# Kernel optimization log

Measured on AMD Instinct MI355X. Metric: run time of the kernel, lower is better.

The kernel has to match this reference:

```python
import jax, jax.numpy as jnp
import numpy as np

EPS = 1e-7  # K.epsilon()

def squash(v, axis=-1):
    s2 = jnp.sum(jnp.square(v), axis=axis, keepdims=True)
    scale = s2 / (1.0 + s2) / jnp.sqrt(s2 + EPS)
    return scale * v

def setup_inputs() -> dict:
    key = jax.random.key(0)
    k1, k2 = jax.random.split(key)
    B, N, D_in = 128, 2048, 8
    J, P = 32, 16
    x = jax.random.normal(k1, (B, N, D_in), dtype=jnp.float32)
    W = jax.random.normal(k2, (J, N, P, D_in), dtype=jnp.float32) * 0.05
    return {"x": x, "W": W}

def reference(x, W):
    # x: [B, N, D_in]; W: [J, N, P, D_in]
    routings = 3
    J = W.shape[0]
    # inputs_hat: [B, J, N, P] -- u_hat_{j|n} = W_{jn} @ u_n
    inputs_hat = jnp.einsum('bni,jnpi->bjnp', x, W)
    B, _, N, _ = inputs_hat.shape
    b = jnp.zeros((B, J, N), dtype=inputs_hat.dtype)
    outputs = None
    for i in range(routings):
        c = jax.nn.softmax(b, axis=1)  # softmax over output capsules J
        s = jnp.einsum('bjn,bjnp->bjp', c, inputs_hat)
        outputs = squash(s)  # [B, J, P]
        if i < routings - 1:
            b = b + jnp.einsum('bjp,bjnp->bjn', outputs, inputs_hat)
    return outputs
```

## Files before the change

### kernel.cpp

```cpp
#include <hip/hip_runtime.h>
#include <math.h>

constexpr int Bb = 128;
constexpr int Nn = 2048;
constexpr int Dd = 8;
constexpr int Jj = 32;
constexpr int Pp = 16;

constexpr int BT = 2;
constexpr int WV = 8;
constexpr int BB = BT * WV;
constexpr int BN = 32;
constexpr int NBC = Bb / BB;
constexpr int NNC = Nn / BN;
constexpr int GRID = NBC * NNC;
constexpr int SZ = Bb * Jj * Pp;
constexpr size_t W16_ELEMS = (size_t)Jj * Nn * Pp * Dd;

typedef _Float16 half2v __attribute__((ext_vector_type(2)));
typedef _Float16 half8  __attribute__((ext_vector_type(8)));
typedef float    floatx4 __attribute__((ext_vector_type(4)));

#if __has_builtin(__builtin_amdgcn_fdot2)
__device__ inline float fdot2(half2v a, half2v b, float c) {
    return __builtin_amdgcn_fdot2(a, b, c, false);
}
#else
__device__ inline float fdot2(half2v a, half2v b, float c) {
    return (float)a.x * (float)b.x + (float)a.y * (float)b.y + c;
}
#endif

__device__ inline half2v bch2(unsigned u) { return __builtin_bit_cast(half2v, u); }
__device__ inline half8  bch8(uint4 u)    { return __builtin_bit_cast(half8, u); }
__device__ inline unsigned pkh2(float lo, float hi) {
    half2v h; h.x = (_Float16)lo; h.y = (_Float16)hi;
    return __builtin_bit_cast(unsigned, h);
}

__global__ __launch_bounds__(256)
void w16cvt_k(const float* __restrict__ W, ushort* __restrict__ W16)
{
    const size_t g = (size_t)blockIdx.x * 256 + threadIdx.x;
    const float4* Wg = reinterpret_cast<const float4*>(W);
    float4 a = Wg[2 * g], b = Wg[2 * g + 1];
    uint4 o;
    o.x = pkh2(a.x, a.y); o.y = pkh2(a.z, a.w);
    o.z = pkh2(b.x, b.y); o.w = pkh2(b.z, b.w);
    reinterpret_cast<uint4*>(W16)[g] = o;
}

__global__ __launch_bounds__(512, 4)
void gemm0_v3(const float* __restrict__ x, const ushort* __restrict__ W16,
              float* __restrict__ S)
{
    __shared__ uint4 xl[32 * 128];

    const int tid  = threadIdx.x;
    const int wave = tid >> 6;
    const int lane = tid & 63;

    const int id  = blockIdx.x;
    const int xcd = id & 7;
    const int rem = id >> 3;
    const int jpc = rem & 7;
    const int nch = rem >> 3;
    const int nc  = xcd + 8 * nch;
    const int jp0 = jpc * 64;
    const int n0  = nc * 32;

    {
        const int xb = tid >> 2, xq = tid & 3;
        const float4* Xg = reinterpret_cast<const float4*>(x);
        #pragma unroll
        for (int r = 0; r < 8; ++r) {
            const int nn = r * 4 + xq;
            const size_t base = ((size_t)xb * 2048 + n0 + nn) * 2;
            float4 a = Xg[base], b = Xg[base + 1];
            uint4 o;
            o.x = pkh2(a.x, a.y); o.y = pkh2(a.z, a.w);
            o.z = pkh2(b.x, b.y); o.w = pkh2(b.z, b.w);
            xl[nn * 128 + xb] = o;
        }
    }
    __syncthreads();

    const int ar = lane & 15;
    const int kg = lane >> 4;

    const uint4* W16v = reinterpret_cast<const uint4*>(W16);
    const size_t abase = ((size_t)(jpc * 4) * 2048 + n0 + kg) * 16 + ar;

    floatx4 acc[4];
    #pragma unroll
    for (int f = 0; f < 4; ++f)
        #pragma unroll
        for (int q = 0; q < 4; ++q) acc[f][q] = 0.f;

    #pragma unroll
    for (int ks = 0; ks < 8; ++ks) {
        half8 bfrag = bch8(xl[(ks * 4 + kg) * 128 + wave * 16 + ar]);
        #pragma unroll
        for (int f = 0; f < 4; ++f) {
            half8 afrag = bch8(W16v[abase + (size_t)f * 2048 * 16 + (size_t)ks * 4 * 16]);
            acc[f] = __builtin_amdgcn_mfma_f32_16x16x32_f16(afrag, bfrag, acc[f], 0, 0, 0);
        }
    }

    float* outp = S + (size_t)nc * SZ;
    const int bcol = wave * 16 + ar;
    #pragma unroll
    for (int f = 0; f < 4; ++f) {
        const size_t off = (size_t)bcol * 512 + jp0 + f * 16 + kg * 4;
        *reinterpret_cast<float4*>(outp + off) =
            make_float4(acc[f][0], acc[f][1], acc[f][2], acc[f][3]);
    }
}

__global__ __launch_bounds__(512, 4)
void route_m(const float* __restrict__ x, const ushort* __restrict__ W16,
             const float* __restrict__ OS, float* __restrict__ S)
{
    __shared__ uint4 xl[16 * 32];
    __shared__ float pl[2][512];

    const int tid  = threadIdx.x;
    const int w    = tid >> 6;
    const int lane = tid & 63;
    const int ar   = lane & 15;
    const int kg   = lane >> 4;

    const int id  = blockIdx.x;
    const int xcd = id & 7;
    const int bc  = (id >> 3) & 7;
    const int nch = id >> 6;
    const int nc  = xcd + 8 * nch;
    const int b0  = bc * 16;
    const int n0  = nc * 32;

    {
        const int b = tid >> 5, n = tid & 31;
        const float4* src = reinterpret_cast<const float4*>(
            x + ((size_t)(b0 + b) * Nn + n0 + n) * Dd);
        float4 a = src[0], c4 = src[1];
        uint4 o;
        o.x = pkh2(a.x, a.y);  o.y = pkh2(a.z, a.w);
        o.z = pkh2(c4.x, c4.y); o.w = pkh2(c4.z, c4.w);
        xl[n * 16 + ((b + n) & 15)] = o;
    }

    float4 o4[4];
    {
        const float4* osv = reinterpret_cast<const float4*>(OS);
        #pragma unroll
        for (int f = 0; f < 4; ++f)
            o4[f] = osv[((size_t)(b0 + ar) * Jj + (w * 4 + f)) * 4 + kg];
    }

    float Sa[4][4];
    #pragma unroll
    for (int f = 0; f < 4; ++f)
        #pragma unroll
        for (int q = 0; q < 4; ++q) Sa[f][q] = 0.f;

    const uint4* W16v = reinterpret_cast<const uint4*>(W16);

    __syncthreads();

    uint4 aw[4];
    #pragma unroll
    for (int f = 0; f < 4; ++f)
        aw[f] = W16v[((size_t)(w * 4 + f) * Nn + n0 + kg) * 16 + ar];

    const half8 hz = {};

    for (int g = 0; g < 8; ++g) {
        const int nl = g * 4;

        half8 bfull = bch8(xl[(nl + kg) * 16 + ((ar + nl + kg) & 15)]);

        floatx4 res[4][4];
        #pragma unroll
        for (int s = 0; s < 4; ++s) {
            half8 bs = (kg == s) ? bfull : hz;
            #pragma unroll
            for (int f = 0; f < 4; ++f) {
                floatx4 z = {0.f, 0.f, 0.f, 0.f};
                res[f][s] = __builtin_amdgcn_mfma_f32_16x16x32_f16(bch8(aw[f]), bs, z, 0, 0, 0);
            }
        }

        if (g < 7) {
            #pragma unroll
            for (int f = 0; f < 4; ++f)
                aw[f] = W16v[((size_t)(w * 4 + f) * Nn + n0 + nl + 4 + kg) * 16 + ar];
        }

        float efs0 = 0.f, efs1 = 0.f, efs2 = 0.f, efs3 = 0.f;
        #pragma unroll
        for (int f = 0; f < 4; ++f) {
            #pragma unroll
            for (int s = 0; s < 4; ++s) {
                float lg = o4[f].x * res[f][s][0];
                lg = fmaf(o4[f].y, res[f][s][1], lg);
                lg = fmaf(o4[f].z, res[f][s][2], lg);
                lg = fmaf(o4[f].w, res[f][s][3], lg);
                lg += __shfl_xor(lg, 16, 64);
                lg += __shfl_xor(lg, 32, 64);
                float ee = __expf(lg);
                res[f][s] = res[f][s] * ee;
                if (s == 0) efs0 += ee; else if (s == 1) efs1 += ee;
                else if (s == 2) efs2 += ee; else efs3 += ee;
            }
        }

        float t01 = (kg & 1) ? efs1 : efs0;
        float t23 = (kg & 1) ? efs3 : efs2;
        float myp = (kg & 2) ? t23 : t01;
        pl[g & 1][w * 64 + lane] = myp;
        __syncthreads();

        float se = 0.f;
        #pragma unroll
        for (int ww = 0; ww < 8; ++ww) se += pl[g & 1][ww * 64 + lane];
        float rse = __builtin_amdgcn_rcpf(se);

        float r1 = __shfl_xor(rse, 16, 64);
        float r2 = __shfl_xor(rse, 32, 64);
        float r3 = __shfl_xor(r1, 32, 64);
        float rs[4];
        #pragma unroll
        for (int s = 0; s < 4; ++s) {
            float a01 = ((s ^ kg) & 1) ? r1 : rse;
            float a23 = ((s ^ kg) & 1) ? r3 : r2;
            rs[s] = ((s ^ kg) & 2) ? a23 : a01;
        }

        #pragma unroll
        for (int f = 0; f < 4; ++f) {
            #pragma unroll
            for (int s = 0; s < 4; ++s) {
                #pragma unroll
                for (int q = 0; q < 4; ++q)
                    Sa[f][q] = fmaf(rs[s], res[f][s][q], Sa[f][q]);
            }
        }
    }

    float* outp = S + (size_t)nc * SZ + (size_t)(b0 + ar) * 512;
    #pragma unroll
    for (int f = 0; f < 4; ++f) {
        *reinterpret_cast<float4*>(outp + (w * 4 + f) * 16 + kg * 4) =
            make_float4(Sa[f][0], Sa[f][1], Sa[f][2], Sa[f][3]);
    }
}

template<int WT>
__global__ __launch_bounds__(512, 2)
void gemm0_k2(const float* __restrict__ x, const float* __restrict__ W,
              ushort* __restrict__ W16, float* __restrict__ S)
{
    __shared__ uint4 wl[2][256];
    __shared__ uint4 xl[2][512];

    const int tid  = threadIdx.x;
    const int wave = tid >> 6;
    const int lane = tid & 63;

    const int id  = blockIdx.x;
    const int xcd = id & 7;
    const int rem = id >> 3;
    const int jpc = rem & 7;
    const int nch = rem >> 3;
    const int nc  = xcd + 8 * nch;
    const int jp0 = jpc * 64;
    const int n0  = nc * 32;

    const int wns = (tid >> 6) & 3;
    const int wjpr = tid & 63;
    const int wjp = jp0 + wjpr, wj = wjp >> 4, wp = wjp & 15;
    const int xb = tid >> 2, xq = tid & 3;

    const float4* Wg = reinterpret_cast<const float4*>(W);
    const float4* Xg = reinterpret_cast<const float4*>(x);
    uint4* W16v = reinterpret_cast<uint4*>(W16);

    float4 wa, wb2, xa, xb2;
    auto load_t = [&](int ks) {
        const int n = n0 + ks * 4;
        if (tid < 256) {
            const size_t base = ((size_t)wj * 2048 + (n + wns)) * 32 + wp * 2;
            wa = Wg[base]; wb2 = Wg[base + 1];
        }
        const size_t xbase = ((size_t)xb * 2048 + n) * 2 + xq * 2;
        xa = Xg[xbase]; xb2 = Xg[xbase + 1];
    };
    auto store_t = [&](int buf, int ks) {
        if (tid < 256) {
            uint4 o;
            o.x = pkh2(wa.x, wa.y);   o.y = pkh2(wa.z, wa.w);
            o.z = pkh2(wb2.x, wb2.y); o.w = pkh2(wb2.z, wb2.w);
            wl[buf][tid] = o;
            if (WT)
                W16v[((size_t)wj * 2048 + (n0 + ks * 4 + wns)) * 16 + wp] = o;
        }
        uint4 o2;
        o2.x = pkh2(xa.x, xa.y);   o2.y = pkh2(xa.z, xa.w);
        o2.z = pkh2(xb2.x, xb2.y); o2.w = pkh2(xb2.z, xb2.w);
        xl[buf][xq * 128 + xb] = o2;
    };

    floatx4 acc[4];
    #pragma unroll
    for (int f = 0; f < 4; ++f)
        #pragma unroll
        for (int q = 0; q < 4; ++q) acc[f][q] = 0.f;

    load_t(0);
    store_t(0, 0);
    __syncthreads();

    const int kg = lane >> 4;
    const int ar = lane & 15;

    for (int ks = 0; ks < 8; ++ks) {
        if (ks < 7) load_t(ks + 1);
        const int buf = ks & 1;

        half8 bfrag = bch8(xl[buf][kg * 128 + wave * 16 + ar]);
        #pragma unroll
        for (int f = 0; f < 4; ++f) {
            half8 afrag = bch8(wl[buf][kg * 64 + f * 16 + ar]);
            acc[f] = __builtin_amdgcn_mfma_f32_16x16x32_f16(afrag, bfrag, acc[f], 0, 0, 0);
        }

        if (ks < 7) {
            store_t(buf ^ 1, ks + 1);
            __syncthreads();
        }
    }

    float* outp = S + (size_t)nc * SZ;
    const int bcol = wave * 16 + ar;
    #pragma unroll
    for (int f = 0; f < 4; ++f) {
        const size_t off = (size_t)bcol * 512 + jp0 + f * 16 + kg * 4;
        *reinterpret_cast<float4*>(outp + off) =
            make_float4(acc[f][0], acc[f][1], acc[f][2], acc[f][3]);
    }
}

template<int LOGITS, int ATOMIC, int W16F>
__global__ __launch_bounds__(512, 4)
void route_k(const float* __restrict__ x, const float* __restrict__ W,
             const ushort* __restrict__ W16,
             const float* __restrict__ OS, float* __restrict__ S)
{
    __shared__ uint4 wbuf[2][512];
    __shared__ uint4 xs[BB * BN];

    const int tid  = threadIdx.x;
    const int wave = tid >> 6;
    const int lane = tid & 63;

    const int id  = blockIdx.x;
    const int xcd = id & 7;
    const int bc  = (id >> 3) & 7;
    const int nch = id >> 6;
    const int nc  = xcd + 8 * nch;
    const int b0  = bc * BB;
    const int n0  = nc * BN;
    const int j   = lane >> 1;
    const int hp  = lane & 1;

    {
        const int b = tid >> 5, n = tid & 31;
        const float4* src = reinterpret_cast<const float4*>(
            x + ((size_t)(b0 + b) * Nn + n0 + n) * Dd);
        float4 a = src[0], c4 = src[1];
        uint4 o;
        o.x = pkh2(a.x, a.y);  o.y = pkh2(a.z, a.w);
        o.z = pkh2(c4.x, c4.y); o.w = pkh2(c4.z, c4.w);
        xs[b * BN + n] = o;
    }

    const float4* Wg = reinterpret_cast<const float4*>(W);
    const int sj = tid >> 4;
    const int sp = tid & 15;
    const int sl = sj * 2 + (sp >> 3);
    const int spp = sp & 7;
    const int wslot = spp * 64 + ((sl + spp) & 63);
    const int ispp = tid >> 6;
    const int isl  = ((tid & 63) - ispp) & 63;
    const int isj  = isl >> 1;
    const int isp  = ((isl & 1) << 3) | ispp;
    const uint4* W16v = reinterpret_cast<const uint4*>(W16);
    const size_t wbase16 = (size_t)isj * 32768 + isp;

    float4 sta, stb;
    uint4 st16;
    auto load_slice = [&](int n) {
        if (W16F) {
            st16 = W16v[wbase16 + (size_t)n * 16];
        } else {
            const size_t base = (size_t)n * 32 + sp * 2 + (size_t)sj * ((size_t)Nn * 32);
            sta = Wg[base];
            stb = Wg[base + 1];
        }
    };
    auto store_slice = [&](int buf) {
        if (W16F) {
            wbuf[buf][tid] = st16;
        } else {
            uint4 o;
            o.x = pkh2(sta.x, sta.y);  o.y = pkh2(sta.z, sta.w);
            o.z = pkh2(stb.x, stb.y);  o.w = pkh2(stb.z, stb.w);
            wbuf[buf][wslot] = o;
        }
    };

    float osum[BT][8];
    if (LOGITS) {
        #pragma unroll
        for (int bb = 0; bb < BT; ++bb) {
            const float4* op = reinterpret_cast<const float4*>(
                OS + ((size_t)(b0 + wave * BT + bb) * Jj + j) * Pp + hp * 8);
            float4 a = op[0], b4 = op[1];
            osum[bb][0] = a.x;  osum[bb][1] = a.y;  osum[bb][2] = a.z;  osum[bb][3] = a.w;
            osum[bb][4] = b4.x; osum[bb][5] = b4.y; osum[bb][6] = b4.z; osum[bb][7] = b4.w;
        }
    }

    float Sa[BT][8];
    #pragma unroll
    for (int bb = 0; bb < BT; ++bb)
        #pragma unroll
        for (int pp = 0; pp < 8; ++pp) Sa[bb][pp] = 0.f;

    load_slice(n0);
    store_slice(0);
    __syncthreads();

    const uint4* xw = xs + (size_t)(wave * BT) * BN;

    for (int nn = 0; nn < BN; ++nn) {
        if (nn + 1 < BN) load_slice(n0 + nn + 1);
        const int buf = nn & 1;

        half2v x01[BT], x23[BT], x45[BT], x67[BT];
        #pragma unroll
        for (int bb = 0; bb < BT; ++bb) {
            uint4 xr = xw[(size_t)bb * BN + nn];
            x01[bb] = bch2(xr.x); x23[bb] = bch2(xr.y);
            x45[bb] = bch2(xr.z); x67[bb] = bch2(xr.w);
        }

        float uh[BT][8];
        #pragma unroll
        for (int pp = 0; pp < 8; ++pp) {
            uint4 wv = wbuf[buf][pp * 64 + ((lane + pp) & 63)];
            half2v w01 = bch2(wv.x), w23 = bch2(wv.y);
            half2v w45 = bch2(wv.z), w67 = bch2(wv.w);
            #pragma unroll
            for (int bb = 0; bb < BT; ++bb) {
                float acc = fdot2(w01, x01[bb], 0.f);
                acc = fdot2(w23, x23[bb], acc);
                acc = fdot2(w45, x45[bb], acc);
                acc = fdot2(w67, x67[bb], acc);
                uh[bb][pp] = acc;
            }
        }

        if (!LOGITS) {
            #pragma unroll
            for (int bb = 0; bb < BT; ++bb)
                #pragma unroll
                for (int pp = 0; pp < 8; ++pp) Sa[bb][pp] += uh[bb][pp];
        } else {
            #pragma unroll
            for (int bb = 0; bb < BT; ++bb) {
                float lg = 0.f;
                #pragma unroll
                for (int pp = 0; pp < 8; ++pp)
                    lg = fmaf(osum[bb][pp], uh[bb][pp], lg);
                lg += __shfl_xor(lg, 1, 64);
                float e = __expf(lg);
                float se = e;
                #pragma unroll
                for (int mk = 2; mk <= 32; mk <<= 1)
                    se += __shfl_xor(se, mk, 64);
                float c = e * __builtin_amdgcn_rcpf(se);
                #pragma unroll
                for (int pp = 0; pp < 8; ++pp)
                    Sa[bb][pp] = fmaf(c, uh[bb][pp], Sa[bb][pp]);
            }
        }

        if (nn + 1 < BN) {
            store_slice((nn + 1) & 1);
            __syncthreads();
        }
    }

    #pragma unroll
    for (int bb = 0; bb < BT; ++bb) {
        const size_t off = ((size_t)(b0 + wave * BT + bb) * Jj + j) * Pp + hp * 8;
        if (ATOMIC) {
            float* spd = S + off;
            #pragma unroll
            for (int pp = 0; pp < 8; ++pp) atomicAdd(spd + pp, Sa[bb][pp]);
        } else {
            float4* dst = reinterpret_cast<float4*>(S + (size_t)nc * SZ + off);
            dst[0] = make_float4(Sa[bb][0], Sa[bb][1], Sa[bb][2], Sa[bb][3]);
            dst[1] = make_float4(Sa[bb][4], Sa[bb][5], Sa[bb][6], Sa[bb][7]);
        }
    }
}

__global__ void reduce_squash_k(const float* __restrict__ Sp, int nparts,
                                float scale, float* __restrict__ OS,
                                float* __restrict__ out, int mode)
{
    const int t = blockIdx.x * 64 + threadIdx.x;
    const float4* sp = reinterpret_cast<const float4*>(Sp);
    float4 a = make_float4(0.f, 0.f, 0.f, 0.f);
    #pragma unroll 8
    for (int s = 0; s < nparts; ++s) {
        float4 v = sp[(size_t)s * (SZ / 4) + t];
        a.x += v.x; a.y += v.y; a.z += v.z; a.w += v.w;
    }
    a.x *= scale; a.y *= scale; a.z *= scale; a.w *= scale;
    float s2 = a.x * a.x + a.y * a.y + a.z * a.z + a.w * a.w;
    s2 += __shfl_xor(s2, 1, 64);
    s2 += __shfl_xor(s2, 2, 64);
    const float g = s2 / ((1.f + s2) * sqrtf(s2 + 1e-7f));
    float4 v = make_float4(g * a.x, g * a.y, g * a.z, g * a.w);
    if (mode == 0) {
        reinterpret_cast<float4*>(OS)[t] = v;
    } else if (mode == 1) {
        float4 o = reinterpret_cast<float4*>(OS)[t];
        o.x += v.x; o.y += v.y; o.z += v.z; o.w += v.w;
        reinterpret_cast<float4*>(OS)[t] = o;
    } else {
        reinterpret_cast<float4*>(out)[t] = v;
    }
}

extern "C" void kernel_launch(void* const* d_in, const int* in_sizes, int n_in,
                              void* d_out, int out_size, void* d_ws, size_t ws_size,
                              hipStream_t stream)
{
    const float* x = (const float*)d_in[0];
    const float* W = (const float*)d_in[1];
    float* out = (float*)d_out;

    const size_t needSp = (size_t)(NNC + 1) * SZ * sizeof(float);
    const bool part  = ws_size >= needSp;
    const bool w16ok = ws_size >= needSp + W16_ELEMS * sizeof(ushort);
    dim3 rg(GRID), rb(512);
    dim3 sg(SZ / 4 / 64), sb(64);

    if (part) {
        float* Sp = (float*)d_ws;
        float* OS = Sp + (size_t)NNC * SZ;
        ushort* W16 = (ushort*)(OS + SZ);

        if (w16ok) {
            const int cvtg = (int)(W16_ELEMS / 8 / 256);
            w16cvt_k<<<dim3(cvtg), dim3(256), 0, stream>>>(W, W16);
            gemm0_v3<<<dim3(512), rb, 0, stream>>>(x, W16, Sp);
            reduce_squash_k<<<sg, sb, 0, stream>>>(Sp, NNC, 1.f / Jj, OS, out, 0);

            route_m<<<rg, rb, 0, stream>>>(x, W16, OS, Sp);
            reduce_squash_k<<<sg, sb, 0, stream>>>(Sp, NNC, 1.f, OS, out, 1);

            route_m<<<rg, rb, 0, stream>>>(x, W16, OS, Sp);
            reduce_squash_k<<<sg, sb, 0, stream>>>(Sp, NNC, 1.f, OS, out, 2);
        } else {
            gemm0_k2<0><<<dim3(512), rb, 0, stream>>>(x, W, nullptr, Sp);
            reduce_squash_k<<<sg, sb, 0, stream>>>(Sp, NNC, 1.f / Jj, OS, out, 0);

            route_k<1, 0, 0><<<rg, rb, 0, stream>>>(x, W, nullptr, OS, Sp);
            reduce_squash_k<<<sg, sb, 0, stream>>>(Sp, NNC, 1.f, OS, out, 1);

            route_k<1, 0, 0><<<rg, rb, 0, stream>>>(x, W, nullptr, OS, Sp);
            reduce_squash_k<<<sg, sb, 0, stream>>>(Sp, NNC, 1.f, OS, out, 2);
        }
    } else {
        float* S  = (float*)d_ws;
        float* OS = S + SZ;
        const size_t Sbytes = (size_t)SZ * sizeof(float);

        hipMemsetAsync(S, 0, Sbytes, stream);
        route_k<0, 1, 0><<<rg, rb, 0, stream>>>(x, W, nullptr, nullptr, S);
        reduce_squash_k<<<sg, sb, 0, stream>>>(S, 1, 1.f / Jj, OS, out, 0);

        hipMemsetAsync(S, 0, Sbytes, stream);
        route_k<1, 1, 0><<<rg, rb, 0, stream>>>(x, W, nullptr, OS, S);
        reduce_squash_k<<<sg, sb, 0, stream>>>(S, 1, 1.f, OS, out, 1);

        hipMemsetAsync(S, 0, Sbytes, stream);
        route_k<1, 1, 0><<<rg, rb, 0, stream>>>(x, W, nullptr, OS, S);
        reduce_squash_k<<<sg, sb, 0, stream>>>(S, 1, 1.f, OS, out, 2);
    }
}
```

Measured before the change: 177.2 us.

## Stage routing W tiles through LDS with async global_load_lds double buffering

The routing kernel used to prefetch W fragments directly into registers. It now issues asynchronous global-to-LDS loads (global_load_lds) into a double-buffered shared tile and reads the MFMA operands from LDS. The aim is to overlap the W fetch for the next group with the current group's compute and to reduce register pressure. In exchange it adds 64 KB of LDS per block and lowers the launch-bounds occupancy hint from 4 to 2. It depends on the existing per-iteration __syncthreads to order the async LDS writes against the reads, and there is no explicit vmcnt wait, so that ordering may be unsafe.

```diff
diff --git a/kernel.cpp b/kernel.cpp
--- a/kernel.cpp
+++ b/kernel.cpp
@@ -36,6 +36,12 @@
 __device__ inline unsigned pkh2(float lo, float hi) {
     half2v h; h.x = (_Float16)lo; h.y = (_Float16)hi;
     return __builtin_bit_cast(unsigned, h);
+}
+
+__device__ inline void gll16(const void* g, void* l) {
+    typedef __attribute__((address_space(1))) const void gvoid;
+    typedef __attribute__((address_space(3))) void lvoid;
+    __builtin_amdgcn_global_load_lds((gvoid*)g, (lvoid*)l, 16, 0, 0);
 }
 
 __global__ __launch_bounds__(256)
@@ -117,10 +123,11 @@
     }
 }
 
-__global__ __launch_bounds__(512, 4)
+__global__ __launch_bounds__(512, 2)
 void route_m(const float* __restrict__ x, const ushort* __restrict__ W16,
              const float* __restrict__ OS, float* __restrict__ S)
 {
+    __shared__ uint4 wl[2][2048];
     __shared__ uint4 xl[16 * 32];
     __shared__ float pl[2][512];
 
@@ -149,6 +156,16 @@
         xl[n * 16 + ((b + n) & 15)] = o;
     }
 
+    {
+        #pragma unroll
+        for (int r = 0; r < 4; ++r) {
+            const int flat = r * 512 + tid;
+            const int jj = flat >> 6, nn2 = (flat >> 4) & 3, pp = flat & 15;
+            const ushort* gp = W16 + (((size_t)jj * Nn + n0 + nn2) * 16 + pp) * 8;
+            gll16(gp, &wl[0][flat]);
+        }
+    }
+
     float4 o4[4];
     {
         const float4* osv = reinterpret_cast<const float4*>(OS);
@@ -163,19 +180,29 @@
         #pragma unroll
         for (int q = 0; q < 4; ++q) Sa[f][q] = 0.f;
 
-    const uint4* W16v = reinterpret_cast<const uint4*>(W16);
-
     __syncthreads();
-
-    uint4 aw[4];
-    #pragma unroll
-    for (int f = 0; f < 4; ++f)
-        aw[f] = W16v[((size_t)(w * 4 + f) * Nn + n0 + kg) * 16 + ar];
 
     const half8 hz = {};
 
     for (int g = 0; g < 8; ++g) {
         const int nl = g * 4;
+        const int buf = g & 1;
+
+        if (g < 7) {
+            #pragma unroll
+            for (int r = 0; r < 4; ++r) {
+                const int flat = r * 512 + tid;
+                const int jj = flat >> 6, nn2 = (flat >> 4) & 3, pp = flat & 15;
+                const ushort* gp = W16 +
+                    (((size_t)jj * Nn + n0 + nl + 4 + nn2) * 16 + pp) * 8;
+                gll16(gp, &wl[buf ^ 1][flat]);
+            }
+        }
+
+        uint4 aw4[4];
+        #pragma unroll
+        for (int f = 0; f < 4; ++f)
+            aw4[f] = wl[buf][(w * 4 + f) * 64 + kg * 16 + ar];
 
         half8 bfull = bch8(xl[(nl + kg) * 16 + ((ar + nl + kg) & 15)]);
 
@@ -186,14 +213,8 @@
             #pragma unroll
             for (int f = 0; f < 4; ++f) {
                 floatx4 z = {0.f, 0.f, 0.f, 0.f};
-                res[f][s] = __builtin_amdgcn_mfma_f32_16x16x32_f16(bch8(aw[f]), bs, z, 0, 0, 0);
+                res[f][s] = __builtin_amdgcn_mfma_f32_16x16x32_f16(bch8(aw4[f]), bs, z, 0, 0, 0);
             }
-        }
-
-        if (g < 7) {
-            #pragma unroll
-            for (int f = 0; f < 4; ++f)
-                aw[f] = W16v[((size_t)(w * 4 + f) * Nn + n0 + nl + 4 + kg) * 16 + ar];
         }
 
         float efs0 = 0.f, efs1 = 0.f, efs2 = 0.f, efs3 = 0.f;
@@ -217,12 +238,12 @@
         float t01 = (kg & 1) ? efs1 : efs0;
         float t23 = (kg & 1) ? efs3 : efs2;
         float myp = (kg & 2) ? t23 : t01;
-        pl[g & 1][w * 64 + lane] = myp;
+        pl[buf][w * 64 + lane] = myp;
         __syncthreads();
 
         float se = 0.f;
         #pragma unroll
-        for (int ww = 0; ww < 8; ++ww) se += pl[g & 1][ww * 64 + lane];
+        for (int ww = 0; ww < 8; ++ww) se += pl[buf][ww * 64 + lane];
         float rse = __builtin_amdgcn_rcpf(se);
 
         float r1 = __shfl_xor(rse, 16, 64);
```

Result: slower. 202.2 us (+14.1%).
